# Optimization experiments

Hardware: AMD Instinct MI355X
Metric: run time of the kernel (lower is better)

## Reference

```python
import jax, jax.numpy as jnp
import numpy as np

TOP_K = 2
EPS = 1e-6

def setup_inputs() -> dict:
    key = jax.random.key(0)
    ks = jax.random.split(key, 6)
    Bt, S, D, E, R = 4, 4096, 1024, 8, 4
    s = lambda d: 1.0 / np.sqrt(d)
    return {
        "x": jax.random.normal(ks[0], (Bt, S, D), jnp.float32),
        "W_base": jax.random.normal(ks[1], (D, D), jnp.float32) * s(D),
        "b_base": jax.random.normal(ks[2], (D,), jnp.float32) * 0.02,
        "W_router": jax.random.normal(ks[3], (E, D), jnp.float32) * s(D),
        "A": jax.random.normal(ks[4], (E, D, R), jnp.float32) * s(D),
        "B": jax.random.normal(ks[5], (E, R, D), jnp.float32) * s(R),
    }

def reference(x, W_base, b_base, W_router, A, B):
    # frozen base linear: [b,s,d] @ [out,d]^T + bias
    base_out = jnp.einsum('bsd,od->bso', x, W_base) + b_base
    # router softmax gate over experts
    logits = jnp.einsum('bsd,ed->bse', x, W_router)
    gate = jax.nn.softmax(logits, axis=-1)
    # top-k scatter-mask (values kept are the gate values themselves)
    topv, topi = jax.lax.top_k(gate, TOP_K)                    # [b,s,k]
    mask = jnp.sum(jax.nn.one_hot(topi, gate.shape[-1], dtype=gate.dtype), axis=-2)
    gate = gate * mask
    gate = gate / (jnp.sum(gate, axis=-1, keepdims=True) + EPS)
    # batched rank-4 LoRA experts, gating applied in low-rank space
    h = jnp.einsum('bsd,edr->bser', x, A)                      # [b,s,E,r]
    hg = h * gate[..., None]                                   # weight before up-proj
    lora_out = jnp.einsum('bser,ero->bso', hg, B)
    return base_out + lora_out
```

## Files before the change

### kernel.cpp

```cpp
#include <hip/hip_runtime.h>
#include <cstdint>

typedef __attribute__((ext_vector_type(8))) short short8;
typedef __attribute__((ext_vector_type(4))) float f32x4;

__device__ inline unsigned short f2bf(float f){
  union { float f; uint32_t u; } v; v.f = f;
  uint32_t r = v.u + 0x7FFFu + ((v.u >> 16) & 1u);
  return (unsigned short)(r >> 16);
}

#define GLL(gp, lp) __builtin_amdgcn_global_load_lds(              \
    (const __attribute__((address_space(1))) void*)(gp),           \
    (__attribute__((address_space(3))) void*)(lp), 16, 0, 0)

__global__ __launch_bounds__(256) void kconv(const float* __restrict__ W,
                                             const float* __restrict__ A,
                                             const float* __restrict__ Bm,
                                             unsigned short* __restrict__ Wb,
                                             unsigned short* __restrict__ BTt,
                                             unsigned short* __restrict__ W2b){
  int i = blockIdx.x * 256 + threadIdx.x;
  Wb[i] = f2bf(W[i]);
  if (i < 32768){
    int o = i >> 5, c = i & 31;
    BTt[i] = f2bf(Bm[(size_t)c*1024 + o]);
    int n = i >> 10, d = i & 1023;
    W2b[i] = f2bf(A[(((size_t)(n>>2))*1024 + d)*4 + (n&3)]);
  }
}

__global__ __launch_bounds__(256) void kxl(const float* __restrict__ x,
                                           const float* __restrict__ Wr,
                                           unsigned short* __restrict__ xb,
                                           float* __restrict__ gate){
  __shared__ float wr[8192];
  const int tid  = threadIdx.x;
  const int lane = tid & 63;
  const int w    = tid >> 6;
  {
    const float4* s  = (const float4*)Wr;
    float4*       d4 = (float4*)wr;
    #pragma unroll
    for (int j=0;j<8;j++) d4[j*256+tid] = s[j*256+tid];
  }
  __syncthreads();
  const float4* wr4 = (const float4*)wr;
  #pragma unroll 1
  for (int tt=0; tt<4; tt++){
    const size_t tok = (size_t)blockIdx.x*16 + w*4 + tt;
    const float4* xr = (const float4*)(x + tok*1024);
    ushort4*      xd = (ushort4*)(xb + tok*1024);
    float4 xv[4];
    #pragma unroll
    for (int c=0;c<4;c++){
      xv[c] = xr[c*64 + lane];
      ushort4 o4; o4.x=f2bf(xv[c].x); o4.y=f2bf(xv[c].y);
      o4.z=f2bf(xv[c].z); o4.w=f2bf(xv[c].w);
      xd[c*64 + lane] = o4;
    }
    float p[8];
    #pragma unroll
    for (int e=0;e<8;e++){
      float a = 0.f;
      #pragma unroll
      for (int c=0;c<4;c++){
        float4 wv = wr4[e*256 + c*64 + lane];
        a += xv[c].x*wv.x + xv[c].y*wv.y + xv[c].z*wv.z + xv[c].w*wv.w;
      }
      p[e] = a;
    }
    #pragma unroll
    for (int off=32; off; off>>=1){
      #pragma unroll
      for (int e=0;e<8;e++) p[e] += __shfl_xor(p[e], off, 64);
    }
    if (lane == 0){
      float mx = p[0];
      #pragma unroll
      for (int e=1;e<8;e++) mx = fmaxf(mx, p[e]);
      float ex[8], s2 = 0.f;
      #pragma unroll
      for (int e=0;e<8;e++){ ex[e] = __expf(p[e]-mx); s2 += ex[e]; }
      int i1 = 0; float v1 = ex[0];
      #pragma unroll
      for (int e=1;e<8;e++) if (ex[e] > v1){ v1 = ex[e]; i1 = e; }
      int i2 = -1; float v2 = -1.f;
      #pragma unroll
      for (int e=0;e<8;e++) if (e != i1 && ex[e] > v2){ v2 = ex[e]; i2 = e; }
      float g1 = v1/s2, g2 = v2/s2;
      float rs = 1.f/(g1 + g2 + 1e-6f);
      float* go = gate + tok*8;
      #pragma unroll
      for (int e=0;e<8;e++) go[e] = (e==i1 ? g1 : (e==i2 ? g2 : 0.f)) * rs;
    }
  }
}

__global__ __launch_bounds__(256) void kh(const unsigned short* __restrict__ xbp,
                                          const unsigned short* __restrict__ W2b,
                                          const float* __restrict__ gate,
                                          unsigned short* __restrict__ HG){
  const int tid  = threadIdx.x;
  const int lane = tid & 63;
  const int wid  = tid >> 6;
  const int lrow = lane & 15;
  const int lk   = (lane >> 4) * 8;
  const int tok0 = blockIdx.x*64 + wid*16;
  f32x4 acc0 = {0.f,0.f,0.f,0.f}, acc1 = {0.f,0.f,0.f,0.f};
  const unsigned short* b0 = W2b + (size_t)lrow*1024 + lk;
  const unsigned short* b1 = W2b + (size_t)(16+lrow)*1024 + lk;
  const unsigned short* ar = xbp + (size_t)(tok0+lrow)*1024 + lk;
  #pragma unroll 4
  for (int ks=0; ks<32; ks++){
    short8 av  = *(const short8*)(ar + ks*32);
    short8 bv0 = *(const short8*)(b0 + ks*32);
    short8 bv1 = *(const short8*)(b1 + ks*32);
    acc0 = __builtin_amdgcn_mfma_f32_16x16x32_bf16(av, bv0, acc0, 0, 0, 0);
    acc1 = __builtin_amdgcn_mfma_f32_16x16x32_bf16(av, bv1, acc1, 0, 0, 0);
  }
  #pragma unroll
  for (int j=0;j<4;j++){
    int tok = tok0 + (lane>>4)*4 + j;
    float g0 = gate[(size_t)tok*8 + (lrow>>2)];
    float g1 = gate[(size_t)tok*8 + 4 + (lrow>>2)];
    HG[(size_t)tok*32 + lrow]      = f2bf(acc0[j]*g0);
    HG[(size_t)tok*32 + 16 + lrow] = f2bf(acc1[j]*g1);
  }
}

__global__ __launch_bounds__(512, 2) void kgemm2(const unsigned short* __restrict__ xb,
                                                 const unsigned short* __restrict__ Wb,
                                                 const unsigned short* __restrict__ BTt,
                                                 const unsigned short* __restrict__ HG,
                                                 const float* __restrict__ bias,
                                                 float* __restrict__ out){
  __shared__ char lds[65536];
  const int tid  = threadIdx.x;
  const int lane = tid & 63;
  const int w    = tid >> 6;
  const int xcd  = blockIdx.x & 7, jj = blockIdx.x >> 3;
  const int nblk = xcd >> 1;
  const int mblk = (xcd & 1) * 32 + jj;
  const int m0 = mblk << 8, n0 = nblk << 8;
  const int wm = w >> 2, wn = w & 3;
  const int lrow = lane & 15;
  const int lkb  = (lane >> 4) << 4;

  int offA[8], offB[4];
  #pragma unroll
  for (int fm=0; fm<8; fm++){ int r = wm*128 + fm*16 + lrow; offA[fm] = r*64 + (lkb ^ (((r>>1)&3)<<4)); }
  #pragma unroll
  for (int fn=0; fn<4; fn++){ int r = wn*64  + fn*16 + lrow; offB[fn] = r*64 + (lkb ^ (((r>>1)&3)<<4)); }

  const int Rb0 = (w&3)*16 + (w>>2)*128 + (lane>>2);
  const int Rb1 = Rb0 + 64;
  const int ob  = (lane&3)*16;
  const int sw0 = ((Rb0>>1)&3)<<4, sw1 = ((Rb1>>1)&3)<<4;
  const char* Ag0 = (const char*)xb + (size_t)(m0+Rb0)*2048 + (ob ^ sw0);
  const char* Ag1 = (const char*)xb + (size_t)(m0+Rb1)*2048 + (ob ^ sw1);
  const char* Bg0 = (const char*)Wb + (size_t)(n0+Rb0)*2048 + (ob ^ sw0);
  const char* Bg1 = (const char*)Wb + (size_t)(n0+Rb1)*2048 + (ob ^ sw1);
  const int dH0 = ((w&3)*16 + (w>>2)*128)*64 + lane*16;
  const int dH1 = dH0 + 4096;

  f32x4 acc[8][4];
  #pragma unroll
  for (int a=0;a<8;a++)
    #pragma unroll
    for (int b=0;b<4;b++) acc[a][b] = (f32x4){0.f,0.f,0.f,0.f};

  GLL(Ag0 +  0, lds + dH0);            GLL(Ag1 +  0, lds + dH1);
  GLL(Bg0 +  0, lds + 32768 + dH0);    GLL(Bg1 +  0, lds + 32768 + dH1);
  GLL(Ag0 + 64, lds + 16384 + dH0);    GLL(Bg0 + 64, lds + 49152 + dH0);

  #pragma unroll 1
  for (int t = 0; t < 32; ++t){
    const int s = t & 1;
    const char* Ab = lds + s*16384;
    const char* Bb = lds + 32768 + s*16384;
    if (t < 31){
      const int s1 = (t+1)&1;
      GLL(Ag1 + (t+1)*64, lds + s1*16384 + dH1);
      GLL(Bg1 + (t+1)*64, lds + 32768 + s1*16384 + dH1);
      asm volatile("s_waitcnt vmcnt(4)" ::: "memory");
    } else {
      asm volatile("s_waitcnt vmcnt(0)" ::: "memory");
    }
    __builtin_amdgcn_s_barrier();
    short8 bf[4];
    #pragma unroll
    for (int fn=0;fn<4;fn++) bf[fn] = *(const short8*)(Bb + offB[fn]);
    short8 af[4];
    #pragma unroll
    for (int fm=0;fm<4;fm++) af[fm] = *(const short8*)(Ab + offA[fm]);
    __builtin_amdgcn_s_setprio(1);
    #pragma unroll
    for (int fm=0;fm<4;fm++)
      #pragma unroll
      for (int fn=0;fn<4;fn++)
        acc[fm][fn] = __builtin_amdgcn_mfma_f32_16x16x32_bf16(af[fm], bf[fn], acc[fm][fn], 0, 0, 0);
    __builtin_amdgcn_s_setprio(0);
    __builtin_amdgcn_s_barrier();
    if (t < 30){
      const int s2 = t & 1;
      GLL(Ag0 + (t+2)*64, lds + s2*16384 + dH0);
      GLL(Bg0 + (t+2)*64, lds + 32768 + s2*16384 + dH0);
    }
    short8 ag[4];
    #pragma unroll
    for (int fm=0;fm<4;fm++) ag[fm] = *(const short8*)(Ab + offA[4+fm]);
    __builtin_amdgcn_s_setprio(1);
    #pragma unroll
    for (int fm=0;fm<4;fm++)
      #pragma unroll
      for (int fn=0;fn<4;fn++)
        acc[4+fm][fn] = __builtin_amdgcn_mfma_f32_16x16x32_bf16(ag[fm], bf[fn], acc[4+fm][fn], 0, 0, 0);
    __builtin_amdgcn_s_setprio(0);
    __builtin_amdgcn_s_barrier();
  }

  {
    const char* Hg0 = (const char*)HG  + (size_t)(m0+Rb0)*64 + (ob ^ sw0);
    const char* Hg1 = (const char*)HG  + (size_t)(m0+Rb1)*64 + (ob ^ sw1);
    const char* Tg0 = (const char*)BTt + (size_t)(n0+Rb0)*64 + (ob ^ sw0);
    const char* Tg1 = (const char*)BTt + (size_t)(n0+Rb1)*64 + (ob ^ sw1);
    GLL(Hg0, lds + dH0);          GLL(Hg1, lds + dH1);
    GLL(Tg0, lds + 32768 + dH0);  GLL(Tg1, lds + 32768 + dH1);
    asm volatile("s_waitcnt vmcnt(0)" ::: "memory");
    __builtin_amdgcn_s_barrier();
    short8 hb[4];
    #pragma unroll
    for (int fn=0;fn<4;fn++) hb[fn] = *(const short8*)(lds + 32768 + offB[fn]);
    #pragma unroll
    for (int fm=0;fm<8;fm++){
      short8 ha = *(const short8*)(lds + offA[fm]);
      #pragma unroll
      for (int fn=0;fn<4;fn++)
        acc[fm][fn] = __builtin_amdgcn_mfma_f32_16x16x32_bf16(ha, hb[fn], acc[fm][fn], 0, 0, 0);
    }
  }

  #pragma unroll
  for (int fn=0;fn<4;fn++){
    int col = n0 + wn*64 + fn*16 + lrow;
    float bv = bias[col];
    #pragma unroll
    for (int fm=0;fm<8;fm++){
      int rb = m0 + wm*128 + fm*16 + (lane>>4)*4;
      #pragma unroll
      for (int j=0;j<4;j++)
        out[(size_t)(rb+j)*1024 + col] = acc[fm][fn][j] + bv;
    }
  }
}

extern "C" void kernel_launch(void* const* d_in, const int* in_sizes, int n_in,
                              void* d_out, int out_size, void* d_ws, size_t ws_size,
                              hipStream_t stream){
  const float* x  = (const float*)d_in[0];
  const float* W  = (const float*)d_in[1];
  const float* bb = (const float*)d_in[2];
  const float* Wr = (const float*)d_in[3];
  const float* A  = (const float*)d_in[4];
  const float* Bm = (const float*)d_in[5];
  float* out = (float*)d_out;
  char* ws = (char*)d_ws;

  unsigned short* Wb   = (unsigned short*)(ws + 0);
  unsigned short* BTt  = (unsigned short*)(ws + 2097152);
  unsigned short* W2b  = (unsigned short*)(ws + 2162688);
  float*          gate = (float*)         (ws + 2228224);
  unsigned short* HG   = (unsigned short*)(ws + 2752512);
  unsigned short* xb   = (unsigned short*)(ws + 3801088);

  kconv<<<4096, 256, 0, stream>>>(W, A, Bm, Wb, BTt, W2b);
  kxl<<<1024, 256, 0, stream>>>(x, Wr, xb, gate);
  kh<<<256, 256, 0, stream>>>(xb, W2b, gate, HG);
  kgemm2<<<256, 512, 0, stream>>>(xb, Wb, BTt, HG, bb, out);
}
```

Measured before the change: 97.46 us.

## Double K-tile depth to 64 in main GEMM with finer-grained staged prefetch

The main bf16 GEMM now processes 64-element K tiles (128-byte rows) instead of 32, halving the number of loop iterations and barrier rounds, with LDS doubled to 128 KB and a new XOR swizzle. Each iteration is split into four MFMA quadrants, and loads of the next B tile and the A tile after it are interleaved between them to overlap global-to-LDS traffic with compute. The 128 KB LDS per block likely limits occupancy to one block per CU despite launch_bounds(512,2), trading latency hiding from occupancy for deeper per-block pipelining.

```diff
diff --git a/kernel.cpp b/kernel.cpp
--- a/kernel.cpp
+++ b/kernel.cpp
@@ -129,40 +129,49 @@
   }
 }
 
-__global__ __launch_bounds__(512, 2) void kgemm2(const unsigned short* __restrict__ xb,
+__global__ __launch_bounds__(512, 2) void kgemm3(const unsigned short* __restrict__ xb,
                                                  const unsigned short* __restrict__ Wb,
                                                  const unsigned short* __restrict__ BTt,
                                                  const unsigned short* __restrict__ HG,
                                                  const float* __restrict__ bias,
                                                  float* __restrict__ out){
-  __shared__ char lds[65536];
+  __shared__ char lds[131072];
+  char* ldsc = lds;
   const int tid  = threadIdx.x;
   const int lane = tid & 63;
   const int w    = tid >> 6;
   const int xcd  = blockIdx.x & 7, jj = blockIdx.x >> 3;
   const int nblk = xcd >> 1;
-  const int mblk = (xcd & 1) * 32 + jj;
+  const int mblk = (xcd & 1)*32 + jj;
   const int m0 = mblk << 8, n0 = nblk << 8;
   const int wm = w >> 2, wn = w & 3;
   const int lrow = lane & 15;
-  const int lkb  = (lane >> 4) << 4;
-
+  const int q    = lane >> 4;
+
+  const int swzk = (lrow & 7) << 4;
   int offA[8], offB[4];
   #pragma unroll
-  for (int fm=0; fm<8; fm++){ int r = wm*128 + fm*16 + lrow; offA[fm] = r*64 + (lkb ^ (((r>>1)&3)<<4)); }
-  #pragma unroll
-  for (int fn=0; fn<4; fn++){ int r = wn*64  + fn*16 + lrow; offB[fn] = r*64 + (lkb ^ (((r>>1)&3)<<4)); }
-
-  const int Rb0 = (w&3)*16 + (w>>2)*128 + (lane>>2);
-  const int Rb1 = Rb0 + 64;
-  const int ob  = (lane&3)*16;
-  const int sw0 = ((Rb0>>1)&3)<<4, sw1 = ((Rb1>>1)&3)<<4;
-  const char* Ag0 = (const char*)xb + (size_t)(m0+Rb0)*2048 + (ob ^ sw0);
-  const char* Ag1 = (const char*)xb + (size_t)(m0+Rb1)*2048 + (ob ^ sw1);
-  const char* Bg0 = (const char*)Wb + (size_t)(n0+Rb0)*2048 + (ob ^ sw0);
-  const char* Bg1 = (const char*)Wb + (size_t)(n0+Rb1)*2048 + (ob ^ sw1);
-  const int dH0 = ((w&3)*16 + (w>>2)*128)*64 + lane*16;
-  const int dH1 = dH0 + 4096;
+  for (int fm=0; fm<8; fm++){ int r = wm*128 + fm*16 + lrow; offA[fm] = r*128 + ((q<<4) ^ swzk); }
+  #pragma unroll
+  for (int fn=0; fn<4; fn++){ int r = wn*64  + fn*16 + lrow; offB[fn] = r*128 + ((q<<4) ^ swzk); }
+
+  const int rowL = lane >> 3;
+  const int colb = ((lane & 7) ^ rowL) << 4;
+  const int rbA = (w>>2)*128 + (w&3)*16;
+  const int rbB = w*16;
+  const char* AgA = (const char*)xb + ((size_t)(m0 + rbA + rowL) << 11) + colb;
+  const char* BgA = (const char*)Wb + ((size_t)(n0 + rbB + rowL) << 11) + colb;
+
+#define STG_A(tt, h, ss) do{                                                        \
+    GLL(AgA + (size_t)(h)*131072 + (tt)*128,                                        \
+        ldsc + (ss)*32768 + (rbA + (h)*64)*128 + lane*16);                          \
+    GLL(AgA + (size_t)(h)*131072 + 16384 + (tt)*128,                                \
+        ldsc + (ss)*32768 + (rbA + (h)*64 + 8)*128 + lane*16); }while(0)
+#define STG_B(tt, h, ss) do{                                                        \
+    GLL(BgA + (size_t)(h)*262144 + (tt)*128,                                        \
+        ldsc + 65536 + (ss)*32768 + (rbB + (h)*128)*128 + lane*16);                 \
+    GLL(BgA + (size_t)(h)*262144 + 16384 + (tt)*128,                                \
+        ldsc + 65536 + (ss)*32768 + (rbB + (h)*128 + 8)*128 + lane*16); }while(0)
 
   f32x4 acc[8][4];
   #pragma unroll
@@ -170,73 +179,116 @@
     #pragma unroll
     for (int b=0;b<4;b++) acc[a][b] = (f32x4){0.f,0.f,0.f,0.f};
 
-  GLL(Ag0 +  0, lds + dH0);            GLL(Ag1 +  0, lds + dH1);
-  GLL(Bg0 +  0, lds + 32768 + dH0);    GLL(Bg1 +  0, lds + 32768 + dH1);
-  GLL(Ag0 + 64, lds + 16384 + dH0);    GLL(Bg0 + 64, lds + 49152 + dH0);
+  STG_A(0,0,0); STG_A(0,1,0); STG_B(0,0,0); STG_B(0,1,0);
+  STG_A(1,0,1); STG_A(1,1,1);
+  asm volatile("s_waitcnt vmcnt(4)" ::: "memory");
+  __builtin_amdgcn_s_barrier();
 
   #pragma unroll 1
-  for (int t = 0; t < 32; ++t){
-    const int s = t & 1;
-    const char* Ab = lds + s*16384;
-    const char* Bb = lds + 32768 + s*16384;
-    if (t < 31){
-      const int s1 = (t+1)&1;
-      GLL(Ag1 + (t+1)*64, lds + s1*16384 + dH1);
-      GLL(Bg1 + (t+1)*64, lds + 32768 + s1*16384 + dH1);
+  for (int t = 0; t < 16; ++t){
+    const int s = t & 1, sn = s ^ 1;
+    const char* Ab = ldsc + s*32768;
+    const char* Bb = ldsc + 65536 + s*32768;
+    short8 a[8], b0[4], b1[4];
+    #pragma unroll
+    for (int fm=0; fm<4; fm++){
+      a[fm*2]   = *(const short8*)(Ab + offA[fm]);
+      a[fm*2+1] = *(const short8*)(Ab + (offA[fm]^64));
+    }
+    #pragma unroll
+    for (int fn=0; fn<2; fn++){
+      b0[fn*2]   = *(const short8*)(Bb + offB[fn]);
+      b0[fn*2+1] = *(const short8*)(Bb + (offB[fn]^64));
+    }
+    if (t < 15) STG_B(t+1, 0, sn);
+    __builtin_amdgcn_s_barrier();
+    __builtin_amdgcn_s_setprio(1);
+    #pragma unroll
+    for (int kk=0;kk<2;kk++)
+      #pragma unroll
+      for (int fm=0;fm<4;fm++)
+        #pragma unroll
+        for (int fn=0;fn<2;fn++)
+          acc[fm][fn] = __builtin_amdgcn_mfma_f32_16x16x32_bf16(a[fm*2+kk], b0[fn*2+kk], acc[fm][fn], 0, 0, 0);
+    __builtin_amdgcn_s_setprio(0);
+    __builtin_amdgcn_s_barrier();
+    #pragma unroll
+    for (int fn=0; fn<2; fn++){
+      b1[fn*2]   = *(const short8*)(Bb + offB[2+fn]);
+      b1[fn*2+1] = *(const short8*)(Bb + (offB[2+fn]^64));
+    }
+    if (t < 15) STG_B(t+1, 1, sn);
+    __builtin_amdgcn_s_barrier();
+    __builtin_amdgcn_s_setprio(1);
+    #pragma unroll
+    for (int kk=0;kk<2;kk++)
+      #pragma unroll
+      for (int fm=0;fm<4;fm++)
+        #pragma unroll
+        for (int fn=0;fn<2;fn++)
+          acc[fm][2+fn] = __builtin_amdgcn_mfma_f32_16x16x32_bf16(a[fm*2+kk], b1[fn*2+kk], acc[fm][2+fn], 0, 0, 0);
+    __builtin_amdgcn_s_setprio(0);
+    __builtin_amdgcn_s_barrier();
+    #pragma unroll
+    for (int fm=0; fm<4; fm++){
+      a[fm*2]   = *(const short8*)(Ab + offA[4+fm]);
+      a[fm*2+1] = *(const short8*)(Ab + (offA[4+fm]^64));
+    }
+    if (t < 14) STG_A(t+2, 0, s);
+    __builtin_amdgcn_s_barrier();
+    __builtin_amdgcn_s_setprio(1);
+    #pragma unroll
+    for (int kk=0;kk<2;kk++)
+      #pragma unroll
+      for (int fm=0;fm<4;fm++)
+        #pragma unroll
+        for (int fn=0;fn<2;fn++)
+          acc[4+fm][2+fn] = __builtin_amdgcn_mfma_f32_16x16x32_bf16(a[fm*2+kk], b1[fn*2+kk], acc[4+fm][2+fn], 0, 0, 0);
+    __builtin_amdgcn_s_setprio(0);
+    __builtin_amdgcn_s_barrier();
+    if (t < 14){
+      STG_A(t+2, 1, s);
       asm volatile("s_waitcnt vmcnt(4)" ::: "memory");
     } else {
       asm volatile("s_waitcnt vmcnt(0)" ::: "memory");
     }
     __builtin_amdgcn_s_barrier();
-    short8 bf[4];
-    #pragma unroll
-    for (int fn=0;fn<4;fn++) bf[fn] = *(const short8*)(Bb + offB[fn]);
-    short8 af[4];
-    #pragma unroll
-    for (int fm=0;fm<4;fm++) af[fm] = *(const short8*)(Ab + offA[fm]);
     __builtin_amdgcn_s_setprio(1);
     #pragma unroll
-    for (int fm=0;fm<4;fm++)
-      #pragma unroll
-      for (int fn=0;fn<4;fn++)
-        acc[fm][fn] = __builtin_amdgcn_mfma_f32_16x16x32_bf16(af[fm], bf[fn], acc[fm][fn], 0, 0, 0);
+    for (int kk=0;kk<2;kk++)
+      #pragma unroll
+      for (int fm=0;fm<4;fm++)
+        #pragma unroll
+        for (int fn=0;fn<2;fn++)
+          acc[4+fm][fn] = __builtin_amdgcn_mfma_f32_16x16x32_bf16(a[fm*2+kk], b0[fn*2+kk], acc[4+fm][fn], 0, 0, 0);
     __builtin_amdgcn_s_setprio(0);
     __builtin_amdgcn_s_barrier();
-    if (t < 30){
-      const int s2 = t & 1;
-      GLL(Ag0 + (t+2)*64, lds + s2*16384 + dH0);
-      GLL(Bg0 + (t+2)*64, lds + 32768 + s2*16384 + dH0);
-    }
-    short8 ag[4];
-    #pragma unroll
-    for (int fm=0;fm<4;fm++) ag[fm] = *(const short8*)(Ab + offA[4+fm]);
-    __builtin_amdgcn_s_setprio(1);
-    #pragma unroll
-    for (int fm=0;fm<4;fm++)
-      #pragma unroll
-      for (int fn=0;fn<4;fn++)
-        acc[4+fm][fn] = __builtin_amdgcn_mfma_f32_16x16x32_bf16(ag[fm], bf[fn], acc[4+fm][fn], 0, 0, 0);
-    __builtin_amdgcn_s_setprio(0);
-    __builtin_amdgcn_s_barrier();
   }
 
   {
-    const char* Hg0 = (const char*)HG  + (size_t)(m0+Rb0)*64 + (ob ^ sw0);
-    const char* Hg1 = (const char*)HG  + (size_t)(m0+Rb1)*64 + (ob ^ sw1);
-    const char* Tg0 = (const char*)BTt + (size_t)(n0+Rb0)*64 + (ob ^ sw0);
-    const char* Tg1 = (const char*)BTt + (size_t)(n0+Rb1)*64 + (ob ^ sw1);
-    GLL(Hg0, lds + dH0);          GLL(Hg1, lds + dH1);
-    GLL(Tg0, lds + 32768 + dH0);  GLL(Tg1, lds + 32768 + dH1);
+    const int colb2 = (((lane & 3) ^ ((lane >> 3) & 3)) << 4);
+    const char* Hg = (const char*)HG  + (size_t)(m0 + w*32 + (lane>>2))*64 + colb2;
+    const char* Tg = (const char*)BTt + (size_t)(n0 + w*32 + (lane>>2))*64 + colb2;
+    const int dst2 = w*2048 + lane*16;
+    GLL(Hg,        ldsc + dst2);
+    GLL(Hg + 1024, ldsc + dst2 + 1024);
+    GLL(Tg,        ldsc + 65536 + dst2);
+    GLL(Tg + 1024, ldsc + 65536 + dst2 + 1024);
     asm volatile("s_waitcnt vmcnt(0)" ::: "memory");
     __builtin_amdgcn_s_barrier();
+    const int swz2 = ((lrow >> 1) & 3) << 4;
     short8 hb[4];
     #pragma unroll
-    for (int fn=0;fn<4;fn++) hb[fn] = *(const short8*)(lds + 32768 + offB[fn]);
-    #pragma unroll
-    for (int fm=0;fm<8;fm++){
-      short8 ha = *(const short8*)(lds + offA[fm]);
-      #pragma unroll
-      for (int fn=0;fn<4;fn++)
+    for (int fn=0; fn<4; fn++){
+      int r = wn*64 + fn*16 + lrow;
+      hb[fn] = *(const short8*)(ldsc + 65536 + r*64 + ((q<<4) ^ swz2));
+    }
+    #pragma unroll
+    for (int fm=0; fm<8; fm++){
+      int r = wm*128 + fm*16 + lrow;
+      short8 ha = *(const short8*)(ldsc + r*64 + ((q<<4) ^ swz2));
+      #pragma unroll
+      for (int fn=0; fn<4; fn++)
         acc[fm][fn] = __builtin_amdgcn_mfma_f32_16x16x32_bf16(ha, hb[fn], acc[fm][fn], 0, 0, 0);
     }
   }
@@ -247,12 +299,14 @@
     float bv = bias[col];
     #pragma unroll
     for (int fm=0;fm<8;fm++){
-      int rb = m0 + wm*128 + fm*16 + (lane>>4)*4;
+      int rb = m0 + wm*128 + fm*16 + q*4;
       #pragma unroll
       for (int j=0;j<4;j++)
         out[(size_t)(rb+j)*1024 + col] = acc[fm][fn][j] + bv;
     }
   }
+#undef STG_A
+#undef STG_B
 }
 
 extern "C" void kernel_launch(void* const* d_in, const int* in_sizes, int n_in,
@@ -277,5 +331,5 @@
   kconv<<<4096, 256, 0, stream>>>(W, A, Bm, Wb, BTt, W2b);
   kxl<<<1024, 256, 0, stream>>>(x, Wr, xb, gate);
   kh<<<256, 256, 0, stream>>>(xb, W2b, gate, HG);
-  kgemm2<<<256, 512, 0, stream>>>(xb, Wb, BTt, HG, bb, out);
-}
+  kgemm3<<<256, 512, 0, stream>>>(xb, Wb, BTt, HG, bb, out);
+}
```

Result: no change. 95.85 us (-1.7%).
